# Kernel optimization log

Hardware: AMD Instinct MI355X
Metric: run time of the kernel (lower is better)

Reference implementation:

```python
import jax, jax.numpy as jnp
import numpy as np

NUM_HEADS = 8


def setup_inputs() -> dict:
    key = jax.random.key(0)
    ks = jax.random.split(key, 5)
    b, c, h, w = 8, 256, 32, 32
    x = jax.random.normal(ks[0], (b, c, h, w), dtype=jnp.float32)
    w_qkv = jax.random.normal(ks[1], (3 * c, c), dtype=jnp.float32) * (c ** -0.5)
    b_qkv = jax.random.normal(ks[2], (3 * c,), dtype=jnp.float32) * 0.02
    w_proj = jax.random.normal(ks[3], (c, c), dtype=jnp.float32) * (c ** -0.5)
    b_proj = jax.random.normal(ks[4], (c,), dtype=jnp.float32) * 0.02
    return {"x": x, "w_qkv": w_qkv, "b_qkv": b_qkv, "w_proj": w_proj, "b_proj": b_proj}


def reference(x, w_qkv, b_qkv, w_proj, b_proj):
    b, c, h, w = x.shape
    nh = NUM_HEADS
    dh = c // nh
    L = h * w
    scale = dh ** -0.5
    # 1x1 conv == per-pixel GEMM
    qkv = jnp.einsum('bchw,oc->bohw', x, w_qkv) + b_qkv[None, :, None, None]
    qkv = qkv.reshape(b, 3, nh, dh, L)
    q, k, v = qkv[:, 0], qkv[:, 1], qkv[:, 2]  # each (b, nh, dh, L)
    attn = jnp.einsum('bhdi,bhdj->bhij', q, k) * scale  # (b, nh, L, L)
    attn = jax.nn.softmax(attn, axis=-1)
    out = jnp.einsum('bhdj,bhij->bhdi', v, attn)  # (b, nh, dh, L)
    out = out.reshape(b, c, h, w)
    proj = jnp.einsum('bchw,oc->bohw', out, w_proj) + b_proj[None, :, None, None]
    return x + proj
```

## Files before the change

kernel.cpp:

```cpp
#include <hip/hip_runtime.h>
#include <math.h>

#define B_   8
#define CIN  256
#define L_   1024
#define NH_  8
#define DH_  32

typedef __attribute__((ext_vector_type(8))) short short8;
typedef __attribute__((ext_vector_type(4))) short short4v;
typedef __attribute__((ext_vector_type(4))) float f32x4;
typedef __attribute__((ext_vector_type(4))) unsigned int uint4v;
typedef __attribute__((ext_vector_type(2))) unsigned int uint2v;

__device__ inline short f2bf_hu(float f) {
    union { float f; unsigned u; } v; v.f = f;
    return (short)((v.u + 0x8000u) >> 16);
}
__device__ inline float bf2f(short s) {
    union { unsigned u; float f; } v; v.u = ((unsigned)(unsigned short)s) << 16;
    return v.f;
}
__device__ inline unsigned pkbf2(float a, float b) {
    union { float f; unsigned u; } x, y; x.f = a; y.f = b;
    return __builtin_amdgcn_perm(y.u + 0x8000u, x.u + 0x8000u, 0x07060302u);
}

__global__ __launch_bounds__(256) void qkv_gemm(
    const float* __restrict__ x, const float* __restrict__ w,
    const float* __restrict__ bias, short* __restrict__ qkvT)
{
    __shared__ short Xs[64][40];
    __shared__ short Wt[128][40];
    const int t = threadIdx.x, lane = t & 63, wv = t >> 6;
    const int n = lane & 15, quad = lane >> 4;
    const int b = blockIdx.z, o0 = blockIdx.y * 128, l0 = blockIdx.x * 64;

    float bias_r[8];
    #pragma unroll
    for (int nf = 0; nf < 8; nf++) bias_r[nf] = bias[o0 + nf * 16 + n];

    f32x4 acc[8];
    #pragma unroll
    for (int nf = 0; nf < 8; nf++) acc[nf] = (f32x4){0.f, 0.f, 0.f, 0.f};

    const int cS = t >> 3, lsS = (t & 7) * 8;

    for (int c0 = 0; c0 < CIN; c0 += 32) {
        {
            const float* xp = &x[(((size_t)b * CIN + c0 + cS) << 10) + l0 + lsS];
            const float4 xa = *(const float4*)xp;
            const float4 xb = *(const float4*)(xp + 4);
            const float vals[8] = {xa.x, xa.y, xa.z, xa.w, xb.x, xb.y, xb.z, xb.w};
            #pragma unroll
            for (int k = 0; k < 8; k++) {
                const int l = lsS + k;
                const int col = (((cS >> 3) ^ (l & 3)) << 3) | (cS & 7);
                Xs[l][col] = f2bf_hu(vals[k]);
            }
        }
        {
            const int o = t >> 1, cs = (t & 1) * 16;
            const float* wp = &w[(size_t)(o0 + o) * CIN + c0 + cs];
            const float4 w0 = *(const float4*)(wp);
            const float4 w1 = *(const float4*)(wp + 4);
            const float4 w2 = *(const float4*)(wp + 8);
            const float4 w3 = *(const float4*)(wp + 12);
            uint4v pa = { pkbf2(w0.x, w0.y), pkbf2(w0.z, w0.w),
                          pkbf2(w1.x, w1.y), pkbf2(w1.z, w1.w) };
            uint4v pb = { pkbf2(w2.x, w2.y), pkbf2(w2.z, w2.w),
                          pkbf2(w3.x, w3.y), pkbf2(w3.z, w3.w) };
            *(uint4v*)&Wt[o][cs]     = pa;
            *(uint4v*)&Wt[o][cs + 8] = pb;
        }
        __syncthreads();

        const int arow = wv * 16 + n;
        const short8 af = *(const short8*)&Xs[arow][(quad ^ (arow & 3)) * 8];
        #pragma unroll
        for (int nf = 0; nf < 8; nf++) {
            const short8 bf = *(const short8*)&Wt[nf * 16 + n][quad * 8];
            acc[nf] = __builtin_amdgcn_mfma_f32_16x16x32_bf16(af, bf, acc[nf], 0, 0, 0);
        }
        __syncthreads();
    }

    #pragma unroll
    for (int reg = 0; reg < 4; reg++) {
        const size_t l = l0 + wv * 16 + quad * 4 + reg;
        short* row = qkvT + (((size_t)b << 10) + l) * 768 + o0 + n;
        #pragma unroll
        for (int nf = 0; nf < 8; nf++)
            row[nf * 16] = f2bf_hu(acc[nf][reg] + bias_r[nf]);
    }
}

__global__ __launch_bounds__(256) void proj_gemm(
    const short* __restrict__ partO, const float* __restrict__ partD,
    const float* __restrict__ w, const float* __restrict__ bias,
    const float* __restrict__ resid, float* __restrict__ out)
{
    __shared__ short Xs[64][40];
    __shared__ short Wt[64][40];
    const int t = threadIdx.x, lane = t & 63, wv = t >> 6;
    const int n = lane & 15, quad = lane >> 4;
    const int b = blockIdx.z, o0 = blockIdx.y * 64, l0 = blockIdx.x * 64;

    float bias_r[4];
    #pragma unroll
    for (int reg = 0; reg < 4; reg++) bias_r[reg] = bias[o0 + wv * 16 + quad * 4 + reg];

    f32x4 acc[4];
    #pragma unroll
    for (int nf = 0; nf < 4; nf++) acc[nf] = (f32x4){0.f, 0.f, 0.f, 0.f};

    for (int c0 = 0; c0 < CIN; c0 += 32) {
        {
            const int l = t >> 2, cs = (t & 3) * 8;
            const int h = c0 >> 5;
            const size_t li = ((size_t)b << 10) + l0 + l;
            const short8 s0 = *(const short8*)&partO[(0 * (size_t)B_ * L_ + li) * CIN + c0 + cs];
            const short8 s1 = *(const short8*)&partO[(1 * (size_t)B_ * L_ + li) * CIN + c0 + cs];
            const float d = partD[(0 * (size_t)B_ * L_ + li) * NH_ + h]
                          + partD[(1 * (size_t)B_ * L_ + li) * NH_ + h];
            const float inv = 1.f / d;
            float v[8];
            #pragma unroll
            for (int e = 0; e < 8; e++) v[e] = (bf2f(s0[e]) + bf2f(s1[e])) * inv;
            uint4v pw = { pkbf2(v[0], v[1]), pkbf2(v[2], v[3]),
                          pkbf2(v[4], v[5]), pkbf2(v[6], v[7]) };
            *(uint4v*)&Xs[l][cs] = pw;
        }
        {
            const int o = t >> 2, cs = (t & 3) * 8;
            const float* wp = &w[(size_t)(o0 + o) * CIN + c0 + cs];
            const float4 a4 = *(const float4*)(wp);
            const float4 b4 = *(const float4*)(wp + 4);
            uint4v pw = { pkbf2(a4.x, a4.y), pkbf2(a4.z, a4.w),
                          pkbf2(b4.x, b4.y), pkbf2(b4.z, b4.w) };
            *(uint4v*)&Wt[o][cs] = pw;
        }
        __syncthreads();

        const short8 af = *(const short8*)&Wt[wv * 16 + n][quad * 8];
        #pragma unroll
        for (int nf = 0; nf < 4; nf++) {
            const short8 bf = *(const short8*)&Xs[nf * 16 + n][quad * 8];
            acc[nf] = __builtin_amdgcn_mfma_f32_16x16x32_bf16(af, bf, acc[nf], 0, 0, 0);
        }
        __syncthreads();
    }

    #pragma unroll
    for (int reg = 0; reg < 4; reg++) {
        const int o = o0 + wv * 16 + quad * 4 + reg;
        #pragma unroll
        for (int nf = 0; nf < 4; nf++) {
            const size_t off = (((size_t)b * CIN + o) << 10) + l0 + nf * 16 + n;
            out[off] = acc[nf][reg] + bias_r[reg] + resid[off];
        }
    }
}

__global__ __launch_bounds__(256) void attn_mfma(
    const short* __restrict__ qkvT, short* __restrict__ partO,
    float* __restrict__ partD)
{
    __shared__ short Vt[2][32][80];
    __shared__ __align__(16) short Ss[128][88];

    const int t = threadIdx.x, lane = t & 63, wv = t >> 6;
    const int n = lane & 15, quad = lane >> 4;
    const int id = blockIdx.x;
    const int bh = id & 63;
    const int b = bh >> 3, h = bh & 7;
    const int i0 = ((id >> 6) & 7) * 128;
    const int s  = id >> 9;

    const short* base = qkvT + ((size_t)b << 10) * 768;

    short8 qa[2];
    #pragma unroll
    for (int a = 0; a < 2; a++)
        qa[a] = *(const short8*)&base[(size_t)(i0 + wv * 32 + a * 16 + n) * 768
                                      + h * DH_ + quad * 8];

    short8 vf2;
    {
        const short one = (n == 0) ? (short)0x3F80 : (short)0;
        #pragma unroll
        for (int u = 0; u < 8; u++) vf2[u] = one;
    }

    f32x4 o_acc[2][3];
    #pragma unroll
    for (int a = 0; a < 2; a++)
        #pragma unroll
        for (int nf = 0; nf < 3; nf++) o_acc[a][nf] = (f32x4){0.f, 0.f, 0.f, 0.f};

    const float K1 = 0.25503510f;
    const float K2 = 11.54156036f;
    const int TSTRIDE = 64 * 768;

    const size_t soff = (size_t)s * 8 * TSTRIDE;
    const short* kp0 = base + 256 + h * DH_ + (size_t)n * 768 + quad * 8 + soff;
    const short* kp1 = kp0 + 16 * 768;
    const short* kp2 = kp0 + 32 * 768;
    const short* kp3 = kp0 + 48 * 768;
    const int jS = t >> 3, dsS = (t & 7) * 4;
    const short* vp0 = base + 512 + h * DH_ + (size_t)jS * 768 + dsS + soff;
    const short* vp1 = vp0 + 32 * 768;

    const int vmsk = ((dsS >> 2) & 7) << 3;
    const int vwo0 = dsS * 80 + (jS ^ vmsk);
    const int vwo1 = dsS * 80 + ((jS + 32) ^ vmsk);
    short* const vtb0 = &Vt[0][0][0];
    short* const vtb1 = &Vt[1][0][0];
    short* const ssw  = &Ss[wv * 32 + n][quad * 4];
    const short* const ssr = &Ss[wv * 32 + n][quad * 8];
    int vro[2][2];
    #pragma unroll
    for (int nf = 0; nf < 2; nf++) {
        const int dv = nf * 16 + n;
        const int msk = ((dv >> 2) & 7) << 3;
        #pragma unroll
        for (int kk = 0; kk < 2; kk++)
            vro[kk][nf] = dv * 80 + ((kk * 32 + quad * 8) ^ msk);
    }

    short8 kfA[4], kfB[4];

    auto stageV = [&](short* vtb) {
        const short4v a = *(const short4v*)vp0; vp0 += TSTRIDE;
        const short4v c = *(const short4v*)vp1; vp1 += TSTRIDE;
        #pragma unroll
        for (int u = 0; u < 4; u++) {
            vtb[vwo0 + u * 80] = a[u];
            vtb[vwo1 + u * 80] = c[u];
        }
    };
    auto loadK = [&](short8* kf) {
        kf[0] = *(const short8*)kp0; kp0 += TSTRIDE;
        kf[1] = *(const short8*)kp1; kp1 += TSTRIDE;
        kf[2] = *(const short8*)kp2; kp2 += TSTRIDE;
        kf[3] = *(const short8*)kp3; kp3 += TSTRIDE;
    };
    auto tile = [&](const short8* kf, const short* vtb) {
        #pragma unroll
        for (int f = 0; f < 4; f++) {
            #pragma unroll
            for (int a = 0; a < 2; a++) {
                f32x4 z = {0.f, 0.f, 0.f, 0.f};
                const f32x4 sv = __builtin_amdgcn_mfma_f32_16x16x32_bf16(kf[f], qa[a], z, 0, 0, 0);
                const float p0 = __builtin_amdgcn_exp2f(fmaf(sv[0], K1, -K2));
                const float p1 = __builtin_amdgcn_exp2f(fmaf(sv[1], K1, -K2));
                const float p2 = __builtin_amdgcn_exp2f(fmaf(sv[2], K1, -K2));
                const float p3 = __builtin_amdgcn_exp2f(fmaf(sv[3], K1, -K2));
                uint2v pk = { pkbf2(p0, p1), pkbf2(p2, p3) };
                *(uint2v*)(ssw + a * 16 * 88 + f * 16) = pk;
            }
        }
        #pragma unroll
        for (int kk = 0; kk < 2; kk++) {
            short8 pf[2];
            #pragma unroll
            for (int a = 0; a < 2; a++)
                pf[a] = *(const short8*)(ssr + a * 16 * 88 + kk * 32);
            #pragma unroll
            for (int nf = 0; nf < 2; nf++) {
                const short8 vf = *(const short8*)(vtb + vro[kk][nf]);
                #pragma unroll
                for (int a = 0; a < 2; a++)
                    o_acc[a][nf] = __builtin_amdgcn_mfma_f32_16x16x32_bf16(pf[a], vf, o_acc[a][nf], 0, 0, 0);
            }
            #pragma unroll
            for (int a = 0; a < 2; a++)
                o_acc[a][2] = __builtin_amdgcn_mfma_f32_16x16x32_bf16(pf[a], vf2, o_acc[a][2], 0, 0, 0);
        }
    };

    stageV(vtb0);
    loadK(kfA);

    for (int itp = 0; itp < 4; itp++) {
        __syncthreads();
        stageV(vtb1);
        loadK(kfB);
        tile(kfA, vtb0);
        __syncthreads();
        if (itp < 3) { stageV(vtb0); loadK(kfA); }
        tile(kfB, vtb1);
    }

    #pragma unroll
    for (int a = 0; a < 2; a++) {
        #pragma unroll
        for (int r = 0; r < 4; r++) {
            const int il = i0 + wv * 32 + a * 16 + quad * 4 + r;
            short* po = partO + (((size_t)s * B_ + b) * L_ + il) * CIN + h * DH_;
            po[n]      = f2bf_hu(o_acc[a][0][r]);
            po[16 + n] = f2bf_hu(o_acc[a][1][r]);
        }
    }
    if (n == 0) {
        #pragma unroll
        for (int a = 0; a < 2; a++)
            #pragma unroll
            for (int r = 0; r < 4; r++) {
                const int il = i0 + wv * 32 + a * 16 + quad * 4 + r;
                partD[(((size_t)s * B_ + b) * L_ + il) * NH_ + h] = o_acc[a][2][r];
            }
    }
}

extern "C" void kernel_launch(void* const* d_in, const int* in_sizes, int n_in,
                              void* d_out, int out_size, void* d_ws, size_t ws_size,
                              hipStream_t stream) {
    const float* x      = (const float*)d_in[0];
    const float* w_qkv  = (const float*)d_in[1];
    const float* b_qkv  = (const float*)d_in[2];
    const float* w_proj = (const float*)d_in[3];
    const float* b_proj = (const float*)d_in[4];
    float* out = (float*)d_out;

    short* qkvT  = (short*)d_ws;
    short* partO = qkvT + (size_t)B_ * L_ * 768;
    float* partD = (float*)(partO + (size_t)2 * B_ * L_ * CIN);

    qkv_gemm<<<dim3(16, 6, B_), 256, 0, stream>>>(x, w_qkv, b_qkv, qkvT);
    attn_mfma<<<dim3(1024), 256, 0, stream>>>(qkvT, partO, partD);
    proj_gemm<<<dim3(16, 4, B_), 256, 0, stream>>>(partO, partD, w_proj, b_proj, x, out);
}
```

Before: 112.8 us.

## Pre-convert weights to bf16 and double-buffer GEMM tiles with direct LDS loads

A new wconv kernel converts the QKV and projection weights to bf16 once per call and writes them into the workspace. Both GEMMs then fetch weight tiles with global_load_lds straight into swizzled LDS. Their K loops use double-buffered shared memory, so the next chunk of activations and weights loads while the current MFMAs run, and one barrier per iteration replaces two. The cost is an extra kernel launch, more LDS per block, and a workspace write and read of the converted weights.

Measured after the change: 111.9 us. About the same (-0.8%).

```diff
diff --git a/kernel.cpp b/kernel.cpp
--- a/kernel.cpp
+++ b/kernel.cpp
@@ -25,13 +25,31 @@
     union { float f; unsigned u; } x, y; x.f = a; y.f = b;
     return __builtin_amdgcn_perm(y.u + 0x8000u, x.u + 0x8000u, 0x07060302u);
 }
+__device__ inline void glds16(const void* g, void* l) {
+    __builtin_amdgcn_global_load_lds(
+        (const __attribute__((address_space(1))) void*)g,
+        (__attribute__((address_space(3))) void*)l, 16, 0, 0);
+}
+
+__global__ __launch_bounds__(256) void wconv(
+    const float* __restrict__ wq, const float* __restrict__ wp,
+    short* __restrict__ w2)
+{
+    const size_t e = ((size_t)blockIdx.x * 256 + threadIdx.x) * 8;
+    const float* src = (e < (size_t)768 * 256) ? wq + e : wp + (e - (size_t)768 * 256);
+    const float4 a = *(const float4*)src;
+    const float4 c = *(const float4*)(src + 4);
+    uint4v pk = { pkbf2(a.x, a.y), pkbf2(a.z, a.w),
+                  pkbf2(c.x, c.y), pkbf2(c.z, c.w) };
+    *(uint4v*)(w2 + e) = pk;
+}
 
 __global__ __launch_bounds__(256) void qkv_gemm(
-    const float* __restrict__ x, const float* __restrict__ w,
+    const float* __restrict__ x, const short* __restrict__ w2,
     const float* __restrict__ bias, short* __restrict__ qkvT)
 {
-    __shared__ short Xs[64][40];
-    __shared__ short Wt[128][40];
+    __shared__ __align__(16) short Xs[2][64][40];
+    __shared__ __align__(16) short Wt[2][128][32];
     const int t = threadIdx.x, lane = t & 63, wv = t >> 6;
     const int n = lane & 15, quad = lane >> 4;
     const int b = blockIdx.z, o0 = blockIdx.y * 128, l0 = blockIdx.x * 64;
@@ -46,43 +64,57 @@
 
     const int cS = t >> 3, lsS = (t & 7) * 8;
 
-    for (int c0 = 0; c0 < CIN; c0 += 32) {
-        {
-            const float* xp = &x[(((size_t)b * CIN + c0 + cS) << 10) + l0 + lsS];
-            const float4 xa = *(const float4*)xp;
-            const float4 xb = *(const float4*)(xp + 4);
-            const float vals[8] = {xa.x, xa.y, xa.z, xa.w, xb.x, xb.y, xb.z, xb.w};
-            #pragma unroll
-            for (int k = 0; k < 8; k++) {
-                const int l = lsS + k;
-                const int col = (((cS >> 3) ^ (l & 3)) << 3) | (cS & 7);
-                Xs[l][col] = f2bf_hu(vals[k]);
-            }
-        }
-        {
-            const int o = t >> 1, cs = (t & 1) * 16;
-            const float* wp = &w[(size_t)(o0 + o) * CIN + c0 + cs];
-            const float4 w0 = *(const float4*)(wp);
-            const float4 w1 = *(const float4*)(wp + 4);
-            const float4 w2 = *(const float4*)(wp + 8);
-            const float4 w3 = *(const float4*)(wp + 12);
-            uint4v pa = { pkbf2(w0.x, w0.y), pkbf2(w0.z, w0.w),
-                          pkbf2(w1.x, w1.y), pkbf2(w1.z, w1.w) };
-            uint4v pb = { pkbf2(w2.x, w2.y), pkbf2(w2.z, w2.w),
-                          pkbf2(w3.x, w3.y), pkbf2(w3.z, w3.w) };
-            *(uint4v*)&Wt[o][cs]     = pa;
-            *(uint4v*)&Wt[o][cs + 8] = pb;
-        }
+    const int oA = wv * 32 + (lane >> 2);
+    const int cc = (lane & 3) ^ ((oA >> 1) & 3);
+    const short* wpA = w2 + (size_t)(o0 + oA) * 256 + cc * 8;
+    const short* wpB = wpA + 16 * 256;
+    short* const ldsW0 = &Wt[0][0][0] + wv * 1024;
+    short* const ldsW1 = &Wt[1][0][0] + wv * 1024;
+
+    auto xwrite = [&](int buf, const float4& a, const float4& c) {
+        const float vals[8] = {a.x, a.y, a.z, a.w, c.x, c.y, c.z, c.w};
+        #pragma unroll
+        for (int k = 0; k < 8; k++) {
+            const int ll = lsS + k;
+            const int col = (((cS >> 3) ^ (ll & 3)) << 3) | (cS & 7);
+            Xs[buf][ll][col] = f2bf_hu(vals[k]);
+        }
+    };
+
+    const float* xp = &x[(((size_t)b * CIN + cS) << 10) + l0 + lsS];
+    float4 xa = *(const float4*)xp, xb = *(const float4*)(xp + 4);
+    glds16(wpA, ldsW0);
+    glds16(wpB, ldsW0 + 512);
+    xwrite(0, xa, xb);
+    xp += (size_t)32 << 10;
+    xa = *(const float4*)xp; xb = *(const float4*)(xp + 4);
+
+    const int wsw = (quad ^ ((n >> 1) & 3)) * 8;
+    const int arow = wv * 16 + n;
+    const int xsw = (quad ^ (arow & 3)) * 8;
+
+    #pragma unroll
+    for (int it = 0; it < 8; it++) {
+        const int cur = it & 1;
         __syncthreads();
-
-        const int arow = wv * 16 + n;
-        const short8 af = *(const short8*)&Xs[arow][(quad ^ (arow & 3)) * 8];
+        if (it < 7) {
+            short* ldsn = (cur ? ldsW0 : ldsW1);
+            glds16(wpA + (it + 1) * 32, ldsn);
+            glds16(wpB + (it + 1) * 32, ldsn + 512);
+        }
+        const short8 af = *(const short8*)&Xs[cur][arow][xsw];
         #pragma unroll
         for (int nf = 0; nf < 8; nf++) {
-            const short8 bf = *(const short8*)&Wt[nf * 16 + n][quad * 8];
+            const short8 bf = *(const short8*)&Wt[cur][nf * 16 + n][wsw];
             acc[nf] = __builtin_amdgcn_mfma_f32_16x16x32_bf16(af, bf, acc[nf], 0, 0, 0);
         }
-        __syncthreads();
+        if (it < 7) {
+            xwrite(cur ^ 1, xa, xb);
+            if (it < 6) {
+                xp += (size_t)32 << 10;
+                xa = *(const float4*)xp; xb = *(const float4*)(xp + 4);
+            }
+        }
     }
 
     #pragma unroll
@@ -97,11 +129,11 @@
 
 __global__ __launch_bounds__(256) void proj_gemm(
     const short* __restrict__ partO, const float* __restrict__ partD,
-    const float* __restrict__ w, const float* __restrict__ bias,
+    const short* __restrict__ w2, const float* __restrict__ bias,
     const float* __restrict__ resid, float* __restrict__ out)
 {
-    __shared__ short Xs[64][40];
-    __shared__ short Wt[64][40];
+    __shared__ __align__(16) short Xs[2][64][40];
+    __shared__ __align__(16) short Wt[2][64][32];
     const int t = threadIdx.x, lane = t & 63, wv = t >> 6;
     const int n = lane & 15, quad = lane >> 4;
     const int b = blockIdx.z, o0 = blockIdx.y * 64, l0 = blockIdx.x * 64;
@@ -114,41 +146,59 @@
     #pragma unroll
     for (int nf = 0; nf < 4; nf++) acc[nf] = (f32x4){0.f, 0.f, 0.f, 0.f};
 
-    for (int c0 = 0; c0 < CIN; c0 += 32) {
-        {
-            const int l = t >> 2, cs = (t & 3) * 8;
-            const int h = c0 >> 5;
-            const size_t li = ((size_t)b << 10) + l0 + l;
-            const short8 s0 = *(const short8*)&partO[(0 * (size_t)B_ * L_ + li) * CIN + c0 + cs];
-            const short8 s1 = *(const short8*)&partO[(1 * (size_t)B_ * L_ + li) * CIN + c0 + cs];
-            const float d = partD[(0 * (size_t)B_ * L_ + li) * NH_ + h]
-                          + partD[(1 * (size_t)B_ * L_ + li) * NH_ + h];
-            const float inv = 1.f / d;
-            float v[8];
-            #pragma unroll
-            for (int e = 0; e < 8; e++) v[e] = (bf2f(s0[e]) + bf2f(s1[e])) * inv;
-            uint4v pw = { pkbf2(v[0], v[1]), pkbf2(v[2], v[3]),
-                          pkbf2(v[4], v[5]), pkbf2(v[6], v[7]) };
-            *(uint4v*)&Xs[l][cs] = pw;
-        }
-        {
-            const int o = t >> 2, cs = (t & 3) * 8;
-            const float* wp = &w[(size_t)(o0 + o) * CIN + c0 + cs];
-            const float4 a4 = *(const float4*)(wp);
-            const float4 b4 = *(const float4*)(wp + 4);
-            uint4v pw = { pkbf2(a4.x, a4.y), pkbf2(a4.z, a4.w),
-                          pkbf2(b4.x, b4.y), pkbf2(b4.z, b4.w) };
-            *(uint4v*)&Wt[o][cs] = pw;
-        }
+    const int l = t >> 2, cs = (t & 3) * 8;
+    const size_t li = ((size_t)b << 10) + l0 + l;
+    const short* p0 = &partO[(0 * (size_t)B_ * L_ + li) * CIN + cs];
+    const short* p1 = &partO[(1 * (size_t)B_ * L_ + li) * CIN + cs];
+    const float* pd0 = &partD[(0 * (size_t)B_ * L_ + li) * NH_];
+    const float* pd1 = &partD[(1 * (size_t)B_ * L_ + li) * NH_];
+
+    const int og = wv * 16 + (lane >> 2);
+    const int ccg = (lane & 3) ^ ((og >> 1) & 3);
+    const short* wp = w2 + (size_t)(o0 + og) * 256 + ccg * 8;
+    short* const ldsW0 = &Wt[0][0][0] + wv * 512;
+    short* const ldsW1 = &Wt[1][0][0] + wv * 512;
+
+    short8 s0, s1;
+    float d0, d1;
+    auto combine_write = [&](int buf) {
+        const float inv = 1.f / (d0 + d1);
+        float v[8];
+        #pragma unroll
+        for (int e = 0; e < 8; e++) v[e] = (bf2f(s0[e]) + bf2f(s1[e])) * inv;
+        uint4v pw = { pkbf2(v[0], v[1]), pkbf2(v[2], v[3]),
+                      pkbf2(v[4], v[5]), pkbf2(v[6], v[7]) };
+        *(uint4v*)&Xs[buf][l][cs] = pw;
+    };
+
+    s0 = *(const short8*)p0; s1 = *(const short8*)p1;
+    d0 = pd0[0]; d1 = pd1[0];
+    glds16(wp, ldsW0);
+    combine_write(0);
+    p0 += 32; p1 += 32;
+    s0 = *(const short8*)p0; s1 = *(const short8*)p1;
+    d0 = pd0[1]; d1 = pd1[1];
+
+    const int wsw = (quad ^ ((n >> 1) & 3)) * 8;
+    #pragma unroll
+    for (int it = 0; it < 8; it++) {
+        const int cur = it & 1;
         __syncthreads();
-
-        const short8 af = *(const short8*)&Wt[wv * 16 + n][quad * 8];
+        if (it < 7) glds16(wp + (it + 1) * 32, cur ? ldsW0 : ldsW1);
+        const short8 af = *(const short8*)&Wt[cur][wv * 16 + n][wsw];
         #pragma unroll
         for (int nf = 0; nf < 4; nf++) {
-            const short8 bf = *(const short8*)&Xs[nf * 16 + n][quad * 8];
+            const short8 bf = *(const short8*)&Xs[cur][nf * 16 + n][quad * 8];
             acc[nf] = __builtin_amdgcn_mfma_f32_16x16x32_bf16(af, bf, acc[nf], 0, 0, 0);
         }
-        __syncthreads();
+        if (it < 7) {
+            combine_write(cur ^ 1);
+            if (it < 6) {
+                p0 += 32; p1 += 32;
+                s0 = *(const short8*)p0; s1 = *(const short8*)p1;
+                d0 = pd0[it + 2]; d1 = pd1[it + 2];
+            }
+        }
     }
 
     #pragma unroll
@@ -326,8 +376,11 @@
     short* qkvT  = (short*)d_ws;
     short* partO = qkvT + (size_t)B_ * L_ * 768;
     float* partD = (float*)(partO + (size_t)2 * B_ * L_ * CIN);
-
-    qkv_gemm<<<dim3(16, 6, B_), 256, 0, stream>>>(x, w_qkv, b_qkv, qkvT);
+    short* w2    = (short*)(partD + (size_t)2 * B_ * L_ * NH_);
+
+    wconv<<<dim3(128), 256, 0, stream>>>(w_qkv, w_proj, w2);
+    qkv_gemm<<<dim3(16, 6, B_), 256, 0, stream>>>(x, w2, b_qkv, qkvT);
     attn_mfma<<<dim3(1024), 256, 0, stream>>>(qkvT, partO, partD);
-    proj_gemm<<<dim3(16, 4, B_), 256, 0, stream>>>(partO, partD, w_proj, b_proj, x, out);
-}
+    proj_gemm<<<dim3(16, 4, B_), 256, 0, stream>>>(partO, partD, w2 + (size_t)768 * 256,
+                                                   b_proj, x, out);
+}
```
